# Optimization experiments

Hardware: AMD Instinct MI355X
Metric: run time of the kernel (lower is better)

## Reference

```python
import jax, jax.numpy as jnp
import numpy as np

N, H, B = 1048576, 128, 4096


def setup_inputs() -> dict:
    key = jax.random.key(0)
    ks = jax.random.split(key, 10)
    x = jax.random.normal(ks[0], (N, H), dtype=jnp.float32)
    # sorted segment ids with every segment nonempty (matches torch.bincount/split usage)
    batch = jnp.sort(jnp.concatenate([
        jnp.arange(B, dtype=jnp.int32),
        jax.random.randint(ks[1], (N - B,), 0, B, dtype=jnp.int32),
    ]))
    s = 1.0 / np.sqrt(H)
    u = lambda k, shp: jax.random.uniform(k, shp, jnp.float32, -s, s)
    return {
        'session_embedding': x,
        'batch': batch,
        'W1': u(ks[2], (H, H)), 'b1': u(ks[3], (H,)),
        'W2': u(ks[4], (H, H)), 'b2': u(ks[5], (H,)),
        'Wq': u(ks[6], (1, H)), 'bq': u(ks[7], (1,)),
        'W3': u(ks[8], (H, 2 * H)), 'b3': u(ks[9], (H,)),
    }


def reference(session_embedding, batch, W1, b1, W2, b2, Wq, bq, W3, b3):
    # index of the last node in each session (batch is sorted)
    last_idx = jax.ops.segment_max(jnp.arange(N, dtype=jnp.int32), batch, num_segments=B)  # [B]
    v_n = session_embedding[last_idx]                      # [B, H]
    v_n_rep = v_n[batch]                                   # [N, H] last-node broadcast per node
    # attention logits: q(sigmoid(W1 v_n + W2 v_i))
    gate = jax.nn.sigmoid(v_n_rep @ W1.T + b1 + session_embedding @ W2.T + b2)  # [N, H]
    alpha = gate @ Wq.T + bq                               # [N, 1]
    s_g = jax.ops.segment_sum(alpha * session_embedding, batch, num_segments=B)  # [B, H]
    s_h = jnp.concatenate([v_n, s_g], axis=1) @ W3.T + b3  # [B, H]
    return s_h
```

## Files before the change

### kernel.cpp

```cpp
#include <hip/hip_runtime.h>
#include <hip/hip_bf16.h>

#define N_NODES 1048576
#define H 128
#define B_SESS 4096
#define TILE 128

typedef __attribute__((ext_vector_type(8))) short bf16x8;
typedef __attribute__((ext_vector_type(4))) short bf16x4;
typedef __attribute__((ext_vector_type(4))) float f32x4;

__device__ inline unsigned short f2bf(float f) {
  unsigned int u = __float_as_uint(f);
  u += 0x7FFFu + ((u >> 16) & 1u);
  return (unsigned short)(u >> 16);
}

__global__ void k_w2(const float* __restrict__ W2, unsigned short* __restrict__ W2b) {
  int i = blockIdx.x * 256 + threadIdx.x;
  float4 v = *reinterpret_cast<const float4*>(W2 + (size_t)i * 4);
  bf16x4 o;
  o[0] = (short)f2bf(v.x); o[1] = (short)f2bf(v.y);
  o[2] = (short)f2bf(v.z); o[3] = (short)f2bf(v.w);
  *reinterpret_cast<bf16x4*>(W2b + (size_t)i * 4) = o;
}

__global__ void k_last(const int* __restrict__ batch, int* __restrict__ last_idx) {
  int i = blockIdx.x * blockDim.x + threadIdx.x;
  if (i < N_NODES) {
    if (i == N_NODES - 1 || batch[i] != batch[i + 1]) last_idx[batch[i]] = i;
  }
}

__global__ void k_apre(const float* __restrict__ x, const int* __restrict__ last_idx,
                       const float* __restrict__ W1, const float* __restrict__ b1,
                       const float* __restrict__ b2, float* __restrict__ A_pre) {
  __shared__ float Wl[128][132];
  __shared__ float vn[8][128];
  int t = threadIdx.x;
  for (int i = 0; i < 16; ++i) {
    int e = (t + i * 256) * 4;
    int r = e >> 7, c = e & 127;
    float4 v = *reinterpret_cast<const float4*>(W1 + e);
    Wl[r][c] = v.x; Wl[r][c + 1] = v.y; Wl[r][c + 2] = v.z; Wl[r][c + 3] = v.w;
  }
  int b0 = blockIdx.x * 8;
  for (int i = t; i < 8 * 128; i += 256) {
    int s = i >> 7, c = i & 127;
    vn[s][c] = x[(size_t)last_idx[b0 + s] * H + c];
  }
  __syncthreads();
  int h = t & 127, si = t >> 7;
  float bias = b1[h] + b2[h];
  for (int s = si; s < 8; s += 2) {
    float acc = bias;
    #pragma unroll
    for (int k = 0; k < 128; k += 4) {
      float4 w = *reinterpret_cast<const float4*>(&Wl[h][k]);
      acc += vn[s][k] * w.x + vn[s][k + 1] * w.y + vn[s][k + 2] * w.z + vn[s][k + 3] * w.w;
    }
    A_pre[(size_t)(b0 + s) * H + h] = acc;
  }
}

__launch_bounds__(512)
__global__ void k_main(const float* __restrict__ x, const int* __restrict__ batch,
                       const unsigned short* __restrict__ W2b, const float* __restrict__ Wq,
                       const float* __restrict__ bq, const float* __restrict__ A_pre,
                       float* __restrict__ s_g) {
  __shared__ unsigned short Wl[128][136];
  __shared__ unsigned short Xl[TILE][136];
  __shared__ float alph[TILE];
  __shared__ int bseg[TILE + 1];
  __shared__ float wq[128];
  int t = threadIdx.x;
  int node0 = blockIdx.x * TILE;

  #pragma unroll
  for (int i = 0; i < 8; ++i) {
    int e = (t + i * 512) * 4;
    int r = e >> 7, c = e & 127;
    float4 v = *reinterpret_cast<const float4*>(x + (size_t)node0 * H + e);
    bf16x4 o;
    o[0] = (short)f2bf(v.x); o[1] = (short)f2bf(v.y);
    o[2] = (short)f2bf(v.z); o[3] = (short)f2bf(v.w);
    *reinterpret_cast<bf16x4*>(&Xl[r][c]) = o;
  }
  #pragma unroll
  for (int i = 0; i < 4; ++i) {
    int e = (t + i * 512) * 8;
    int r = e >> 7, c = e & 127;
    *reinterpret_cast<bf16x8*>(&Wl[r][c]) = *reinterpret_cast<const bf16x8*>(W2b + e);
  }
  if (t <= TILE) {
    int idx = node0 + t;
    bseg[t] = (idx < N_NODES) ? batch[idx] : -1;
  }
  if (t < 128) wq[t] = Wq[t];
  __syncthreads();

  int w = t >> 6, lane = t & 63, r = lane & 15, ks = lane >> 4;
  f32x4 acc[8];
  #pragma unroll
  for (int nt = 0; nt < 8; ++nt) acc[nt] = (f32x4){0.f, 0.f, 0.f, 0.f};
  #pragma unroll
  for (int k0 = 0; k0 < 128; k0 += 32) {
    bf16x8 a = *reinterpret_cast<const bf16x8*>(&Xl[w * 16 + r][k0 + ks * 8]);
    #pragma unroll
    for (int nt = 0; nt < 8; ++nt) {
      bf16x8 b = *reinterpret_cast<const bf16x8*>(&Wl[nt * 16 + r][k0 + ks * 8]);
      acc[nt] = __builtin_amdgcn_mfma_f32_16x16x32_bf16(a, b, acc[nt], 0, 0, 0);
    }
  }
  float bqv = bq[0];
  #pragma unroll
  for (int j = 0; j < 4; ++j) {
    int lrow = w * 16 + ks * 4 + j;
    const float* ap = A_pre + (size_t)bseg[lrow] * H;
    float pa = 0.f;
    #pragma unroll
    for (int nt = 0; nt < 8; ++nt) {
      float z = acc[nt][j] + ap[nt * 16 + r];
      float g = 1.0f / (1.0f + __expf(-z));
      pa += g * wq[nt * 16 + r];
    }
    pa += __shfl_xor(pa, 1);
    pa += __shfl_xor(pa, 2);
    pa += __shfl_xor(pa, 4);
    pa += __shfl_xor(pa, 8);
    if (r == 0) alph[lrow] = pa + bqv;
  }
  __syncthreads();

  int h = t & 127, grp = t >> 7;
  int base = grp * 32;
  float accum = 0.f;
  #pragma unroll 4
  for (int n = 0; n < 32; ++n) {
    int ln = base + n;
    float xv = __uint_as_float((unsigned int)Xl[ln][h] << 16);
    accum += alph[ln] * xv;
    if (bseg[ln] != bseg[ln + 1]) {
      atomicAdd(&s_g[(size_t)bseg[ln] * H + h], accum);
      accum = 0.f;
    }
  }
  if (accum != 0.f) atomicAdd(&s_g[(size_t)bseg[base + 31] * H + h], accum);
}

__global__ void k_final(const float* __restrict__ x, const int* __restrict__ last_idx,
                        const float* __restrict__ s_g, const float* __restrict__ W3,
                        const float* __restrict__ b3, float* __restrict__ out) {
  __shared__ float Wl[128][132];
  __shared__ float vin[8][256];
  int t = threadIdx.x;
  int b0 = blockIdx.x * 8;
  for (int i = t; i < 8 * 256; i += 256) {
    int s = i >> 8, c = i & 255;
    float v;
    if (c < 128) v = x[(size_t)last_idx[b0 + s] * H + c];
    else         v = s_g[(size_t)(b0 + s) * H + (c - 128)];
    vin[s][c] = v;
  }
  int h = t & 127, si = t >> 7;
  float res[4];
  for (int half = 0; half < 2; ++half) {
    __syncthreads();
    for (int i = 0; i < 16; ++i) {
      int e = (t + i * 256) * 4;
      int r = e >> 7, c = e & 127;
      float4 v = *reinterpret_cast<const float4*>(W3 + (size_t)r * 256 + half * 128 + c);
      Wl[r][c] = v.x; Wl[r][c + 1] = v.y; Wl[r][c + 2] = v.z; Wl[r][c + 3] = v.w;
    }
    __syncthreads();
    #pragma unroll
    for (int sI = 0; sI < 4; ++sI) {
      int s = si + sI * 2;
      float acc = 0.f;
      #pragma unroll
      for (int k = 0; k < 128; k += 4) {
        float4 wv = *reinterpret_cast<const float4*>(&Wl[h][k]);
        acc += vin[s][half * 128 + k] * wv.x + vin[s][half * 128 + k + 1] * wv.y +
               vin[s][half * 128 + k + 2] * wv.z + vin[s][half * 128 + k + 3] * wv.w;
      }
      if (half == 0) res[sI] = acc;
      else out[(size_t)(b0 + s) * H + h] = res[sI] + acc + b3[h];
    }
  }
}

extern "C" void kernel_launch(void* const* d_in, const int* in_sizes, int n_in,
                              void* d_out, int out_size, void* d_ws, size_t ws_size,
                              hipStream_t stream) {
  const float* x     = (const float*)d_in[0];
  const int*   batch = (const int*)d_in[1];
  const float* W1    = (const float*)d_in[2];
  const float* b1    = (const float*)d_in[3];
  const float* W2    = (const float*)d_in[4];
  const float* b2    = (const float*)d_in[5];
  const float* Wq    = (const float*)d_in[6];
  const float* bq    = (const float*)d_in[7];
  const float* W3    = (const float*)d_in[8];
  const float* b3    = (const float*)d_in[9];
  float* out = (float*)d_out;

  char* ws = (char*)d_ws;
  int*            last_idx = (int*)ws;
  float*          A_pre    = (float*)(ws + 16384);
  float*          s_g      = (float*)(ws + 16384 + 2097152);
  unsigned short* W2b      = (unsigned short*)(ws + 16384 + 2 * 2097152);

  hipMemsetAsync(s_g, 0, (size_t)B_SESS * H * sizeof(float), stream);
  k_w2<<<16, 256, 0, stream>>>(W2, W2b);
  k_last<<<N_NODES / 256, 256, 0, stream>>>(batch, last_idx);
  k_apre<<<B_SESS / 8, 256, 0, stream>>>(x, last_idx, W1, b1, b2, A_pre);
  k_main<<<N_NODES / TILE, 512, 0, stream>>>(x, batch, W2b, Wq, bq, A_pre, s_g);
  k_final<<<B_SESS / 8, 256, 0, stream>>>(x, last_idx, s_g, W3, b3, out);
}
```

Before: 232.4 us.

## Make k_main persistent with double-buffered register prefetch and XOR-swizzled LDS

The main kernel now launches 256 persistent blocks, each looping over 32 node tiles. W2 is staged into LDS once per block instead of once per tile. The next tile's x and segment ids are prefetched into registers while the current tile runs its MFMA and reduction, then written to a second LDS buffer. LDS padding is replaced by an XOR swizzle, with W2 pre-swizzled on the device. The aim is to hide global load latency and amortise setup, at the cost of much higher register pressure from the prefetch and fewer blocks to fill the GPU (256 blocks on a chip with 256 CUs).

```diff
diff --git a/kernel.cpp b/kernel.cpp
--- a/kernel.cpp
+++ b/kernel.cpp
@@ -5,6 +5,8 @@
 #define H 128
 #define B_SESS 4096
 #define TILE 128
+#define NBLOCKS 256
+#define TILES_PER_BLOCK (N_NODES / TILE / NBLOCKS)
 
 typedef __attribute__((ext_vector_type(8))) short bf16x8;
 typedef __attribute__((ext_vector_type(4))) short bf16x4;
@@ -16,13 +18,22 @@
   return (unsigned short)(u >> 16);
 }
 
-__global__ void k_w2(const float* __restrict__ W2, unsigned short* __restrict__ W2b) {
+__device__ inline int swz(int r, int c) {
+  return r * 128 + (((c >> 3) ^ (r & 7)) << 3) + (c & 7);
+}
+
+__global__ void k_w2(const float* __restrict__ W2, unsigned short* __restrict__ W2s) {
   int i = blockIdx.x * 256 + threadIdx.x;
-  float4 v = *reinterpret_cast<const float4*>(W2 + (size_t)i * 4);
-  bf16x4 o;
-  o[0] = (short)f2bf(v.x); o[1] = (short)f2bf(v.y);
-  o[2] = (short)f2bf(v.z); o[3] = (short)f2bf(v.w);
-  *reinterpret_cast<bf16x4*>(W2b + (size_t)i * 4) = o;
+  int r = i >> 4, u = i & 15;
+  const float* src = W2 + (size_t)r * 128 + u * 8;
+  float4 a = *reinterpret_cast<const float4*>(src);
+  float4 b = *reinterpret_cast<const float4*>(src + 4);
+  bf16x8 o;
+  o[0] = (short)f2bf(a.x); o[1] = (short)f2bf(a.y);
+  o[2] = (short)f2bf(a.z); o[3] = (short)f2bf(a.w);
+  o[4] = (short)f2bf(b.x); o[5] = (short)f2bf(b.y);
+  o[6] = (short)f2bf(b.z); o[7] = (short)f2bf(b.w);
+  *reinterpret_cast<bf16x8*>(W2s + r * 128 + (((u ^ (r & 7))) << 3)) = o;
 }
 
 __global__ void k_last(const int* __restrict__ batch, int* __restrict__ last_idx) {
@@ -65,87 +76,135 @@
 
 __launch_bounds__(512)
 __global__ void k_main(const float* __restrict__ x, const int* __restrict__ batch,
-                       const unsigned short* __restrict__ W2b, const float* __restrict__ Wq,
+                       const unsigned short* __restrict__ W2s, const float* __restrict__ Wq,
                        const float* __restrict__ bq, const float* __restrict__ A_pre,
                        float* __restrict__ s_g) {
-  __shared__ unsigned short Wl[128][136];
-  __shared__ unsigned short Xl[TILE][136];
+  __shared__ unsigned short Wl[128 * 128];
+  __shared__ unsigned short Xl[2][TILE * 128];
   __shared__ float alph[TILE];
-  __shared__ int bseg[TILE + 1];
+  __shared__ int bseg[2][TILE + 1];
   __shared__ float wq[128];
+
   int t = threadIdx.x;
-  int node0 = blockIdx.x * TILE;
-
-  #pragma unroll
-  for (int i = 0; i < 8; ++i) {
-    int e = (t + i * 512) * 4;
-    int r = e >> 7, c = e & 127;
-    float4 v = *reinterpret_cast<const float4*>(x + (size_t)node0 * H + e);
-    bf16x4 o;
-    o[0] = (short)f2bf(v.x); o[1] = (short)f2bf(v.y);
-    o[2] = (short)f2bf(v.z); o[3] = (short)f2bf(v.w);
-    *reinterpret_cast<bf16x4*>(&Xl[r][c]) = o;
-  }
   #pragma unroll
   for (int i = 0; i < 4; ++i) {
     int e = (t + i * 512) * 8;
-    int r = e >> 7, c = e & 127;
-    *reinterpret_cast<bf16x8*>(&Wl[r][c]) = *reinterpret_cast<const bf16x8*>(W2b + e);
-  }
-  if (t <= TILE) {
-    int idx = node0 + t;
-    bseg[t] = (idx < N_NODES) ? batch[idx] : -1;
+    *reinterpret_cast<bf16x8*>(&Wl[e]) = *reinterpret_cast<const bf16x8*>(W2s + e);
   }
   if (t < 128) wq[t] = Wq[t];
+  float bqv = bq[0];
+
+  int tile0 = blockIdx.x * TILES_PER_BLOCK;
+  int w = t >> 6, lane = t & 63, r = lane & 15, ks = lane >> 4;
+  int arow = w * 16 + r;
+
+  {
+    size_t base = (size_t)tile0 * TILE * H;
+    float4 h4[8];
+    #pragma unroll
+    for (int i = 0; i < 8; ++i)
+      h4[i] = *reinterpret_cast<const float4*>(x + base + (size_t)(i * 512 + t) * 4);
+    int bv = 0;
+    if (t <= TILE) {
+      int idx = tile0 * TILE + t;
+      bv = (idx < N_NODES) ? batch[idx] : -1;
+    }
+    #pragma unroll
+    for (int i = 0; i < 8; ++i) {
+      int e = (i * 512 + t) * 4;
+      int rr = e >> 7, c = e & 127;
+      bf16x4 o;
+      o[0] = (short)f2bf(h4[i].x); o[1] = (short)f2bf(h4[i].y);
+      o[2] = (short)f2bf(h4[i].z); o[3] = (short)f2bf(h4[i].w);
+      *reinterpret_cast<bf16x4*>(&Xl[0][swz(rr, c)]) = o;
+    }
+    if (t <= TILE) bseg[0][t] = bv;
+  }
   __syncthreads();
 
-  int w = t >> 6, lane = t & 63, r = lane & 15, ks = lane >> 4;
-  f32x4 acc[8];
-  #pragma unroll
-  for (int nt = 0; nt < 8; ++nt) acc[nt] = (f32x4){0.f, 0.f, 0.f, 0.f};
-  #pragma unroll
-  for (int k0 = 0; k0 < 128; k0 += 32) {
-    bf16x8 a = *reinterpret_cast<const bf16x8*>(&Xl[w * 16 + r][k0 + ks * 8]);
-    #pragma unroll
-    for (int nt = 0; nt < 8; ++nt) {
-      bf16x8 b = *reinterpret_cast<const bf16x8*>(&Wl[nt * 16 + r][k0 + ks * 8]);
-      acc[nt] = __builtin_amdgcn_mfma_f32_16x16x32_bf16(a, b, acc[nt], 0, 0, 0);
-    }
-  }
-  float bqv = bq[0];
-  #pragma unroll
-  for (int j = 0; j < 4; ++j) {
-    int lrow = w * 16 + ks * 4 + j;
-    const float* ap = A_pre + (size_t)bseg[lrow] * H;
-    float pa = 0.f;
-    #pragma unroll
-    for (int nt = 0; nt < 8; ++nt) {
-      float z = acc[nt][j] + ap[nt * 16 + r];
-      float g = 1.0f / (1.0f + __expf(-z));
-      pa += g * wq[nt * 16 + r];
-    }
-    pa += __shfl_xor(pa, 1);
-    pa += __shfl_xor(pa, 2);
-    pa += __shfl_xor(pa, 4);
-    pa += __shfl_xor(pa, 8);
-    if (r == 0) alph[lrow] = pa + bqv;
-  }
-  __syncthreads();
-
-  int h = t & 127, grp = t >> 7;
-  int base = grp * 32;
-  float accum = 0.f;
-  #pragma unroll 4
-  for (int n = 0; n < 32; ++n) {
-    int ln = base + n;
-    float xv = __uint_as_float((unsigned int)Xl[ln][h] << 16);
-    accum += alph[ln] * xv;
-    if (bseg[ln] != bseg[ln + 1]) {
-      atomicAdd(&s_g[(size_t)bseg[ln] * H + h], accum);
-      accum = 0.f;
-    }
-  }
-  if (accum != 0.f) atomicAdd(&s_g[(size_t)bseg[base + 31] * H + h], accum);
+  for (int it = 0; it < TILES_PER_BLOCK; ++it) {
+    int cur = it & 1, nxt = cur ^ 1;
+    int node0 = (tile0 + it) * TILE;
+
+    float4 h4[8];
+    int bv = 0;
+    bool pre = (it + 1 < TILES_PER_BLOCK);
+    if (pre) {
+      size_t base = (size_t)(node0 + TILE) * H;
+      #pragma unroll
+      for (int i = 0; i < 8; ++i)
+        h4[i] = *reinterpret_cast<const float4*>(x + base + (size_t)(i * 512 + t) * 4);
+      if (t <= TILE) {
+        int idx = node0 + TILE + t;
+        bv = (idx < N_NODES) ? batch[idx] : -1;
+      }
+    }
+
+    f32x4 acc[8];
+    #pragma unroll
+    for (int nt = 0; nt < 8; ++nt) acc[nt] = (f32x4){0.f, 0.f, 0.f, 0.f};
+    #pragma unroll
+    for (int k0 = 0; k0 < 128; k0 += 32) {
+      int u = (k0 >> 3) + ks;
+      bf16x8 a = *reinterpret_cast<const bf16x8*>(&Xl[cur][arow * 128 + ((u ^ (arow & 7)) << 3)]);
+      #pragma unroll
+      for (int nt = 0; nt < 8; ++nt) {
+        bf16x8 b = *reinterpret_cast<const bf16x8*>(&Wl[(nt * 16 + r) * 128 + ((u ^ (r & 7)) << 3)]);
+        acc[nt] = __builtin_amdgcn_mfma_f32_16x16x32_bf16(a, b, acc[nt], 0, 0, 0);
+      }
+    }
+    #pragma unroll
+    for (int j = 0; j < 4; ++j) {
+      int lrow = w * 16 + ks * 4 + j;
+      const float* ap = A_pre + (size_t)bseg[cur][lrow] * H;
+      float pa = 0.f;
+      #pragma unroll
+      for (int nt = 0; nt < 8; ++nt) {
+        float z = acc[nt][j] + ap[nt * 16 + r];
+        float g = 1.0f / (1.0f + __expf(-z));
+        pa += g * wq[nt * 16 + r];
+      }
+      pa += __shfl_xor(pa, 1);
+      pa += __shfl_xor(pa, 2);
+      pa += __shfl_xor(pa, 4);
+      pa += __shfl_xor(pa, 8);
+      if (r == 0) alph[lrow] = pa + bqv;
+    }
+    __syncthreads();
+
+    {
+      int h = t & 127, grp = t >> 7;
+      int base = grp * 32;
+      int hu = h >> 3, hl = h & 7;
+      float accum = 0.f;
+      #pragma unroll 8
+      for (int n = 0; n < 32; ++n) {
+        int ln = base + n;
+        unsigned short xs = Xl[cur][ln * 128 + (((hu ^ (ln & 7))) << 3) + hl];
+        float xv = __uint_as_float((unsigned int)xs << 16);
+        accum += alph[ln] * xv;
+        if (bseg[cur][ln] != bseg[cur][ln + 1]) {
+          atomicAdd(&s_g[(size_t)bseg[cur][ln] * H + h], accum);
+          accum = 0.f;
+        }
+      }
+      if (accum != 0.f) atomicAdd(&s_g[(size_t)bseg[cur][base + 31] * H + h], accum);
+    }
+
+    if (pre) {
+      #pragma unroll
+      for (int i = 0; i < 8; ++i) {
+        int e = (i * 512 + t) * 4;
+        int rr = e >> 7, c = e & 127;
+        bf16x4 o;
+        o[0] = (short)f2bf(h4[i].x); o[1] = (short)f2bf(h4[i].y);
+        o[2] = (short)f2bf(h4[i].z); o[3] = (short)f2bf(h4[i].w);
+        *reinterpret_cast<bf16x4*>(&Xl[nxt][swz(rr, c)]) = o;
+      }
+      if (t <= TILE) bseg[nxt][t] = bv;
+    }
+    __syncthreads();
+  }
 }
 
 __global__ void k_final(const float* __restrict__ x, const int* __restrict__ last_idx,
@@ -208,12 +267,12 @@
   int*            last_idx = (int*)ws;
   float*          A_pre    = (float*)(ws + 16384);
   float*          s_g      = (float*)(ws + 16384 + 2097152);
-  unsigned short* W2b      = (unsigned short*)(ws + 16384 + 2 * 2097152);
+  unsigned short* W2s      = (unsigned short*)(ws + 16384 + 2 * 2097152);
 
   hipMemsetAsync(s_g, 0, (size_t)B_SESS * H * sizeof(float), stream);
-  k_w2<<<16, 256, 0, stream>>>(W2, W2b);
+  k_w2<<<8, 256, 0, stream>>>(W2, W2s);
   k_last<<<N_NODES / 256, 256, 0, stream>>>(batch, last_idx);
   k_apre<<<B_SESS / 8, 256, 0, stream>>>(x, last_idx, W1, b1, b2, A_pre);
-  k_main<<<N_NODES / TILE, 512, 0, stream>>>(x, batch, W2b, Wq, bq, A_pre, s_g);
+  k_main<<<NBLOCKS, 512, 0, stream>>>(x, batch, W2s, Wq, bq, A_pre, s_g);
   k_final<<<B_SESS / 8, 256, 0, stream>>>(x, last_idx, s_g, W3, b3, out);
 }
```

Measured after the change: 289.2 us. 24.5% more time.
